# Kernel optimization log

Measured on AMD Instinct MI355X. Metric: run time of the kernel, lower is better.

Reference implementation:

```python
import jax, jax.numpy as jnp
import numpy as np

N_EMBD = 1024
HEAD_SIZE = 128
B, T = 8, 4096


def setup_inputs() -> dict:
    key = jax.random.key(0)
    ks = jax.random.split(key, 7)
    s = 1.0 / np.sqrt(N_EMBD)
    return {
        "x": jax.random.normal(ks[0], (B, T, N_EMBD), dtype=jnp.float32),
        "Wq": jax.random.uniform(ks[1], (N_EMBD, HEAD_SIZE), jnp.float32, -s, s),
        "bq": jax.random.uniform(ks[2], (HEAD_SIZE,), jnp.float32, -s, s),
        "Wk": jax.random.uniform(ks[3], (N_EMBD, HEAD_SIZE), jnp.float32, -s, s),
        "bk": jax.random.uniform(ks[4], (HEAD_SIZE,), jnp.float32, -s, s),
        "Wv": jax.random.uniform(ks[5], (N_EMBD, HEAD_SIZE), jnp.float32, -s, s),
        "bv": jax.random.uniform(ks[6], (HEAD_SIZE,), jnp.float32, -s, s),
    }


def reference(x, Wq, bq, Wk, bk, Wv, bv):
    # q,k,v: [B,T,H]
    q = x @ Wq + bq
    k = x @ Wk + bk
    v = x @ Wv + bv
    scale = HEAD_SIZE ** -0.5
    att = jnp.einsum("bth,bsh->bts", q, k) * scale  # [B,T,T]
    t = x.shape[1]
    causal = jnp.tril(jnp.ones((t, t), dtype=bool))
    att = jnp.where(causal, att, -jnp.inf)
    att = jax.nn.softmax(att, axis=-1)
    # dropout with p=0.0 is identity (eval-mode equivalent)
    out = jnp.einsum("bts,bsh->bth", att, v)  # [B,T,H]
    return out
```

## Files before the change

### kernel.cpp

```cpp
#include <hip/hip_runtime.h>
#include <hip/hip_bf16.h>
#include <stdint.h>

#define BATCH 8
#define SEQ   4096
#define EMB   1024
#define HD    128
#define NROWS 32768

typedef __attribute__((ext_vector_type(8))) short short8;
typedef __attribute__((ext_vector_type(4))) float f32x4;

__device__ inline unsigned short f2bf(float f) {
    union { float f; unsigned int u; } c; c.f = f;
    unsigned int u = c.u;
    unsigned int r = (u + 0x7fffu + ((u >> 16) & 1u)) >> 16;
    return (unsigned short)r;
}
__device__ inline float bf2f(unsigned short u) {
    union { unsigned int i; float f; } c; c.i = ((unsigned int)u) << 16; return c.f;
}
__device__ inline unsigned int pkbf(float a, float b) {
    __hip_bfloat162 h = __float22bfloat162_rn(make_float2(a, b));
    union { __hip_bfloat162 h; unsigned int u; } c; c.h = h; return c.u;
}

#define GLDS16(gp, lp) __builtin_amdgcn_global_load_lds( \
    (const __attribute__((address_space(1))) void*)(gp), \
    (__attribute__((address_space(3))) void*)(lp), 16, 0, 0)

__device__ inline void decomp(int it, int& b, int& qt, int& kv) {
    b = it / 2112;
    int r = it - b * 2112;
    int q = (int)((__builtin_sqrtf(2.0f * (float)r + 1.0f) - 1.0f) * 0.5f);
    while (2 * (q + 1) * (q + 2) <= r) ++q;
    while (2 * q * (q + 1) > r) --q;
    qt = q;
    kv = r - 2 * q * (q + 1);
}
__device__ inline int base1(int qt) {
    if (qt < 5)  return qt;
    if (qt < 11) return 5 + 2 * (qt - 5);
    if (qt < 16) return 17 + 3 * (qt - 11);
    if (qt < 22) return 32 + 4 * (qt - 16);
    if (qt < 27) return 56 + 5 * (qt - 22);
    return 81 + 6 * (qt - 27);
}

__global__ __launch_bounds__(256) void prep_kernel(
    const float* __restrict__ Wq, const float* __restrict__ bq,
    const float* __restrict__ Wk, const float* __restrict__ bk,
    const float* __restrict__ Wv, const float* __restrict__ bv,
    unsigned short* __restrict__ wt, float* __restrict__ biasc)
{
    const int n = blockIdx.x;
    const int sel = n >> 7, h = n & 127;
    const float* W = (sel == 0) ? Wq : (sel == 1) ? Wk : Wv;
    const int tid = threadIdx.x;
    const int k0 = tid * 4;
    union { unsigned short us[4]; uint2 v; } pk;
#pragma unroll
    for (int u = 0; u < 4; ++u) pk.us[u] = f2bf(W[(size_t)(k0 + u) * HD + h]);
    *(uint2*)&wt[(size_t)n * EMB + k0] = pk.v;
    if (tid == 0) {
        const float* bp = (sel == 0) ? bq : (sel == 1) ? bk : bv;
        biasc[n] = bp[h];
    }
}

__global__ __launch_bounds__(768, 3) void gemm_qkv(
    const float* __restrict__ x, const unsigned short* __restrict__ wt,
    const float* __restrict__ biasc,
    unsigned short* __restrict__ q, unsigned short* __restrict__ kOut,
    unsigned short* __restrict__ vt)
{
    const int m0  = blockIdx.x * 128;
    const int tid = threadIdx.x;
    const int wave = tid >> 6, lane = tid & 63;
    const int quad = lane >> 4, l15 = lane & 15;
    const int wm = (wave >= 6) ? 1 : 0;
    const int wn = wave - wm * 6;

    __shared__ __align__(16) unsigned short As[3][128][40];
    __shared__ __align__(16) unsigned short Bs[3][12288];

    f32x4 acc[4][4];
#pragma unroll
    for (int i = 0; i < 4; ++i)
#pragma unroll
        for (int j = 0; j < 4; ++j) acc[i][j] = (f32x4){0.f, 0.f, 0.f, 0.f};

    const int aactive = (tid < 512);
    const int arow = tid >> 3, akc = (tid & 7) * 4;
    float4 aR0, aR1;

#define LOAD_A(kt)                                                          \
    if (aactive) {                                                          \
        aR0 = *(const float4*)(x + (size_t)(m0 + arow) * EMB + (kt) * 32 + akc);        \
        aR1 = *(const float4*)(x + (size_t)(m0 + arow + 64) * EMB + (kt) * 32 + akc);   \
    }
#define WRITE_A(buf)                                                        \
    if (aactive) {                                                          \
        union { unsigned short us[4]; uint2 v; } p0, p1;                    \
        p0.us[0] = f2bf(aR0.x); p0.us[1] = f2bf(aR0.y);                     \
        p0.us[2] = f2bf(aR0.z); p0.us[3] = f2bf(aR0.w);                     \
        *(uint2*)&As[buf][arow][akc] = p0.v;                                \
        p1.us[0] = f2bf(aR1.x); p1.us[1] = f2bf(aR1.y);                     \
        p1.us[2] = f2bf(aR1.z); p1.us[3] = f2bf(aR1.w);                     \
        *(uint2*)&As[buf][arow + 64][akc] = p1.v;                           \
    }
#define STAGE_B(kt, buf)                                                    \
    {                                                                       \
        _Pragma("unroll")                                                   \
        for (int g = 0; g < 2; ++g) {                                       \
            int s0 = (g * 12 + wave) * 64;                                  \
            int s  = s0 + lane;                                             \
            int n  = s >> 2, c = (s & 3) ^ (n & 3);                         \
            GLDS16(wt + (size_t)n * EMB + (kt) * 32 + c * 8,                \
                   &Bs[buf][s0 * 8]);                                       \
        }                                                                   \
    }
#define VMW2() { asm volatile("s_waitcnt vmcnt(2)" ::: "memory"); __builtin_amdgcn_sched_barrier(0); }
#define VMW0() { asm volatile("s_waitcnt vmcnt(0)" ::: "memory"); __builtin_amdgcn_sched_barrier(0); }
#define GBAR() { asm volatile("s_waitcnt lgkmcnt(0)\n\ts_barrier" ::: "memory"); __builtin_amdgcn_sched_barrier(0); }

    LOAD_A(0);
    STAGE_B(0, 0);
    STAGE_B(1, 1);
    VMW2();
    WRITE_A(0);
    GBAR();

    int cur = 0;
    for (int kt = 0; kt < 32; ++kt) {
        if (kt < 31) LOAD_A(kt + 1);
        if (kt < 30) { int b2 = cur + 2; if (b2 >= 3) b2 -= 3; STAGE_B(kt + 2, b2); }

        short8 af[4], bw[4];
#pragma unroll
        for (int mj = 0; mj < 4; ++mj)
            af[mj] = *(const short8*)&As[cur][wm * 64 + mj * 16 + l15][quad * 8];
#pragma unroll
        for (int ni = 0; ni < 4; ++ni) {
            int n = wn * 64 + ni * 16 + l15;
            bw[ni] = *(const short8*)&Bs[cur][n * 32 + ((quad ^ (n & 3)) << 3)];
        }
#pragma unroll
        for (int ni = 0; ni < 4; ++ni)
#pragma unroll
            for (int mj = 0; mj < 4; ++mj)
                acc[ni][mj] = __builtin_amdgcn_mfma_f32_16x16x32_bf16(
                    bw[ni], af[mj], acc[ni][mj], 0, 0, 0);

        if (kt == 30) { VMW0(); } else { VMW2(); }
        if (kt < 31) {
            int nb = cur + 1; if (nb >= 3) nb -= 3;
            WRITE_A(nb);
            GBAR();
        }
        cur = (cur + 1 < 3) ? cur + 1 : 0;
    }

    const float qscale = 0.08838834764831845f * 1.4426950408889634f;
    const int bb = m0 >> 12;
    const int t0 = m0 & 4095;
    const int mrow0 = m0 + wm * 64;
    const int tl0   = t0 + wm * 64;
#pragma unroll
    for (int ni = 0; ni < 4; ++ni) {
        int colbase = wn * 64 + ni * 16;
        int sel = colbase >> 7;
        int c0 = colbase + quad * 4;
        float4 bv4 = *(const float4*)&biasc[c0];
#pragma unroll
        for (int mj = 0; mj < 4; ++mj) {
            int m = mrow0 + mj * 16 + l15;
            if (sel == 0) {
                union { unsigned short us[4]; uint2 v; } pk;
#pragma unroll
                for (int j = 0; j < 4; ++j)
                    pk.us[j] = f2bf((acc[ni][mj][j] + ((const float*)&bv4)[j]) * qscale);
                *(uint2*)&q[(size_t)m * HD + (c0 & 127)] = pk.v;
            } else if (sel == 1) {
                union { unsigned short us[4]; uint2 v; } pk;
#pragma unroll
                for (int j = 0; j < 4; ++j)
                    pk.us[j] = f2bf(acc[ni][mj][j] + ((const float*)&bv4)[j]);
                *(uint2*)&kOut[(size_t)m * HD + (c0 & 127)] = pk.v;
            } else {
#pragma unroll
                for (int j = 0; j < 4; ++j) {
                    int h = (c0 & 127) + j;
                    vt[((size_t)(bb * 128 + h)) * SEQ + tl0 + mj * 16 + l15] =
                        f2bf(acc[ni][mj][j] + ((const float*)&bv4)[j]);
                }
            }
        }
    }
#undef LOAD_A
#undef WRITE_A
#undef STAGE_B
#undef VMW2
#undef VMW0
#undef GBAR
}

__global__ __launch_bounds__(256, 3) void attn_kernel(
    const unsigned short* __restrict__ q, const unsigned short* __restrict__ k,
    const unsigned short* __restrict__ vt, float* __restrict__ out,
    float* __restrict__ Oseg, float2* __restrict__ ml)
{
    const int rank  = blockIdx.x;
    const int chunk = (rank & 7) * 96 + (rank >> 3);
    const int start = chunk * 22;
    const int iend  = start + 22;

    const int tid  = threadIdx.x;
    const int wave = tid >> 6, lane = tid & 63;
    const int quad = lane >> 4, l15 = lane & 15;

    __shared__ __align__(16) unsigned short Ks[2][4096];
    __shared__ __align__(16) unsigned short Vs[2][4096];

    const int bpa0 = (l15 + 16 * ((2 * quad) & 3)) * 4;
    const int bpa1 = (l15 + 16 * ((2 * quad + 1) & 3)) * 4;

#define STAGE_KV(b_, kv_, buf_)                                              \
    {                                                                        \
        const size_t kb0 = (size_t)(b_) * SEQ + (kv_) * 32;                  \
        const size_t vb0 = (size_t)(b_) * HD * SEQ + (kv_) * 32;             \
        _Pragma("unroll")                                                    \
        for (int g = 0; g < 2; ++g) {                                        \
            int s0 = (g * 4 + wave) * 64;                                    \
            int s  = s0 + lane;                                              \
            int key = s >> 4, c = (s & 15) ^ (key & 15);                     \
            GLDS16(k + (kb0 + key) * HD + c * 8, &Ks[buf_][s0 * 8]);         \
        }                                                                    \
        _Pragma("unroll")                                                    \
        for (int g = 0; g < 2; ++g) {                                        \
            int s0 = (g * 4 + wave) * 64;                                    \
            int s  = s0 + lane;                                              \
            int h = s >> 2, c = (s & 3) ^ ((h >> 2) & 3);                    \
            GLDS16(vt + vb0 + (size_t)h * SEQ + c * 8, &Vs[buf_][s0 * 8]);   \
        }                                                                    \
    }

    int b, qt, kv;
    decomp(start, b, qt, kv);

    short8 qf[2][4];
    f32x4  o[2][8];
    float  m_r[2], l_r[2];
    int    qrow0 = 0;

#define CTX_INIT(b_, q_)                                                     \
    {                                                                        \
        qrow0 = (q_) * 128 + wave * 32;                                      \
        const size_t qoff = (size_t)(b_) * SEQ + qrow0;                      \
        _Pragma("unroll")                                                    \
        for (int mi = 0; mi < 2; ++mi)                                       \
            _Pragma("unroll")                                                \
            for (int kh = 0; kh < 4; ++kh)                                   \
                qf[mi][kh] = *(const short8*)(q + (qoff + mi * 16 + l15) * HD + kh * 32 + quad * 8); \
        _Pragma("unroll")                                                    \
        for (int mi = 0; mi < 2; ++mi) {                                     \
            _Pragma("unroll")                                                \
            for (int hi = 0; hi < 8; ++hi) o[mi][hi] = (f32x4){0.f, 0.f, 0.f, 0.f}; \
            m_r[mi] = -1e30f; l_r[mi] = 0.f;                                 \
        }                                                                    \
    }

#define CTX_FLUSH()                                                          \
    {                                                                        \
        const int I0 = b * 2112 + 2 * qt * (qt + 1);                         \
        const int j  = chunk - I0 / 22;                                      \
        const int rr = wave * 32;                                            \
        float* obase;                                                        \
        if (j == 0) obase = out + ((size_t)b * SEQ + qrow0) * HD;            \
        else obase = Oseg + ((size_t)(b * 112 + base1(qt) + j - 1) * 128 + rr) * HD; \
        const size_t mlb = ((size_t)(b * 32 + qt) * 7 + j) * 128 + rr;       \
        _Pragma("unroll")                                                    \
        for (int mi = 0; mi < 2; ++mi) {                                     \
            if (quad == 0) ml[mlb + mi * 16 + l15] = make_float2(m_r[mi], l_r[mi]); \
            _Pragma("unroll")                                                \
            for (int hi = 0; hi < 8; ++hi)                                   \
                *(f32x4*)&obase[(size_t)(mi * 16 + l15) * HD + hi * 16 + quad * 4] = o[mi][hi]; \
        }                                                                    \
    }

#define SMAX(sarr, mi_, pk_)                                                 \
    {                                                                        \
        float mx = fmaxf(fmaxf(fmaxf(sarr[0][0], sarr[0][1]),               \
                               fmaxf(sarr[0][2], sarr[0][3])),              \
                         fmaxf(fmaxf(sarr[1][0], sarr[1][1]),               \
                               fmaxf(sarr[1][2], sarr[1][3])));             \
        mx = fmaxf(mx, __shfl_xor(mx, 16));                                  \
        mx = fmaxf(mx, __shfl_xor(mx, 32));                                  \
        if (!__all(mx - m_r[mi_] <= 8.0f)) {                                 \
            float mnew = fmaxf(m_r[mi_], mx);                                \
            float alpha = __builtin_amdgcn_exp2f(m_r[mi_] - mnew);           \
            m_r[mi_] = mnew;                                                 \
            l_r[mi_] *= alpha;                                               \
            _Pragma("unroll")                                                \
            for (int hi = 0; hi < 8; ++hi) o[mi_][hi] *= alpha;              \
        }                                                                    \
        const float mcur = m_r[mi_];                                         \
        float rs = 0.f;                                                      \
        _Pragma("unroll")                                                    \
        for (int ni = 0; ni < 2; ++ni) {                                     \
            float p0 = __builtin_amdgcn_exp2f(sarr[ni][0] - mcur);           \
            float p1 = __builtin_amdgcn_exp2f(sarr[ni][1] - mcur);           \
            float p2 = __builtin_amdgcn_exp2f(sarr[ni][2] - mcur);           \
            float p3 = __builtin_amdgcn_exp2f(sarr[ni][3] - mcur);           \
            rs += (p0 + p1) + (p2 + p3);                                     \
            pk_[ni][0] = pkbf(p0, p1);                                       \
            pk_[ni][1] = pkbf(p2, p3);                                       \
        }                                                                    \
        rs += __shfl_xor(rs, 16);                                            \
        rs += __shfl_xor(rs, 32);                                            \
        l_r[mi_] += rs;                                                      \
    }

#define BPERM(pk_, pT_)                                                      \
    {                                                                        \
        union { unsigned int u[4]; short8 s8; } pt;                          \
        unsigned int a0 = (unsigned)__builtin_amdgcn_ds_bpermute(bpa0, (int)pk_[0][0]); \
        unsigned int b0 = (unsigned)__builtin_amdgcn_ds_bpermute(bpa0, (int)pk_[1][0]); \
        pt.u[0] = (quad < 2) ? a0 : b0;                                      \
        unsigned int a1 = (unsigned)__builtin_amdgcn_ds_bpermute(bpa0, (int)pk_[0][1]); \
        unsigned int b1 = (unsigned)__builtin_amdgcn_ds_bpermute(bpa0, (int)pk_[1][1]); \
        pt.u[1] = (quad < 2) ? a1 : b1;                                      \
        unsigned int a2 = (unsigned)__builtin_amdgcn_ds_bpermute(bpa1, (int)pk_[0][0]); \
        unsigned int b2 = (unsigned)__builtin_amdgcn_ds_bpermute(bpa1, (int)pk_[1][0]); \
        pt.u[2] = (quad < 2) ? a2 : b2;                                      \
        unsigned int a3 = (unsigned)__builtin_amdgcn_ds_bpermute(bpa1, (int)pk_[0][1]); \
        unsigned int b3 = (unsigned)__builtin_amdgcn_ds_bpermute(bpa1, (int)pk_[1][1]); \
        pt.u[3] = (quad < 2) ? a3 : b3;                                      \
        pT_ = pt.s8;                                                         \
    }

    STAGE_KV(b, kv, 0);
    CTX_INIT(b, qt);
    int cur = 0;

    for (int it = start; it < iend; ++it) {
        const bool more = (it + 1 < iend);
        int b2 = b, qt2 = qt, kv2 = kv + 1;
        const bool ctxend = (kv2 == 4 * qt + 4);
        if (ctxend) { kv2 = 0; ++qt2; if (qt2 == 32) { qt2 = 0; ++b2; } }

        __syncthreads();
        if (more) STAGE_KV(b2, kv2, cur ^ 1);

        const int key0 = kv * 32;
        if (key0 <= qrow0 + 31) {
            f32x4 s0[2], s1[2];
#pragma unroll
            for (int ni = 0; ni < 2; ++ni) { s0[ni] = (f32x4){0.f,0.f,0.f,0.f}; s1[ni] = (f32x4){0.f,0.f,0.f,0.f}; }
            __builtin_amdgcn_s_setprio(1);
#pragma unroll
            for (int kh = 0; kh < 4; ++kh) {
#pragma unroll
                for (int ni = 0; ni < 2; ++ni) {
                    short8 kf = *(const short8*)&Ks[cur][(ni * 16 + l15) * 128 + (((kh * 4 + quad) ^ l15) << 3)];
                    s0[ni] = __builtin_amdgcn_mfma_f32_16x16x32_bf16(kf, qf[0][kh], s0[ni], 0, 0, 0);
                    s1[ni] = __builtin_amdgcn_mfma_f32_16x16x32_bf16(kf, qf[1][kh], s1[ni], 0, 0, 0);
                }
            }
            __builtin_amdgcn_s_setprio(0);
            if (key0 + 31 > qrow0) {
#pragma unroll
                for (int ni = 0; ni < 2; ++ni)
#pragma unroll
                    for (int j = 0; j < 4; ++j) {
                        int key = key0 + ni * 16 + quad * 4 + j;
                        if (key > qrow0 + l15)      s0[ni][j] = -1e30f;
                        if (key > qrow0 + 16 + l15) s1[ni][j] = -1e30f;
                    }
            }
            unsigned int pk0[2][2], pk1[2][2];
            short8 pT0, pT1;
            SMAX(s0, 0, pk0)
            BPERM(pk0, pT0)
            SMAX(s1, 1, pk1)
            BPERM(pk1, pT1)
            __builtin_amdgcn_s_setprio(1);
#pragma unroll
            for (int hi = 0; hi < 8; ++hi) {
                short8 vf = *(const short8*)&Vs[cur][(hi * 16 + l15) * 32 + ((quad ^ (l15 >> 2)) << 3)];
                o[0][hi] = __builtin_amdgcn_mfma_f32_16x16x32_bf16(vf, pT0, o[0][hi], 0, 0, 0);
                o[1][hi] = __builtin_amdgcn_mfma_f32_16x16x32_bf16(vf, pT1, o[1][hi], 0, 0, 0);
            }
            __builtin_amdgcn_s_setprio(0);
        }

        if (ctxend || !more) {
            CTX_FLUSH();
            if (more && ctxend) CTX_INIT(b2, qt2);
        }
        b = b2; qt = qt2; kv = kv2;
        cur ^= 1;
    }
#undef STAGE_KV
#undef CTX_INIT
#undef CTX_FLUSH
#undef SMAX
#undef BPERM
}

__global__ __launch_bounds__(256) void merge_kernel(
    float* __restrict__ out, const float* __restrict__ Oseg,
    const float2* __restrict__ ml)
{
    int idx = blockIdx.x * 256 + threadIdx.x;
    int row = idx >> 5;
    int hc  = (idx & 31) << 2;
    int b = row >> 12, t = row & 4095, qt = t >> 7, rr = t & 127;
    int I0   = b * 2112 + 2 * qt * (qt + 1);
    int n    = 4 * (qt + 1);
    int nseg = (I0 + n - 1) / 22 - I0 / 22 + 1;

    const float2* mlp = ml + ((size_t)(b * 32 + qt) * 7) * 128 + rr;
    float2 s0 = mlp[0];
    float M = s0.x;
    for (int j = 1; j < nseg; ++j) M = fmaxf(M, mlp[(size_t)j * 128].x);

    float w0 = __builtin_amdgcn_exp2f(s0.x - M);
    float L  = w0 * s0.y;
    f32x4 a = *(const f32x4*)&out[(size_t)row * HD + hc];
    a = a * w0;
    for (int j = 1; j < nseg; ++j) {
        float2 mj = mlp[(size_t)j * 128];
        float w = __builtin_amdgcn_exp2f(mj.x - M);
        L += w * mj.y;
        const float* sp = Oseg + ((size_t)(b * 112 + base1(qt) + j - 1) * 128 + rr) * HD + hc;
        f32x4 sv = *(const f32x4*)sp;
        a = a + sv * w;
    }
    float inv = 1.0f / L;
    *(f32x4*)&out[(size_t)row * HD + hc] = a * inv;
}

extern "C" void kernel_launch(void* const* d_in, const int* in_sizes, int n_in,
                              void* d_out, int out_size, void* d_ws, size_t ws_size,
                              hipStream_t stream) {
    const float* x  = (const float*)d_in[0];
    const float* Wq = (const float*)d_in[1];
    const float* bq = (const float*)d_in[2];
    const float* Wk = (const float*)d_in[3];
    const float* bk = (const float*)d_in[4];
    const float* Wv = (const float*)d_in[5];
    const float* bv = (const float*)d_in[6];
    float* out = (float*)d_out;

    unsigned short* wt    = (unsigned short*)d_ws;
    float*          biasc = (float*)((char*)d_ws + 786432);
    unsigned short* qb    = (unsigned short*)((char*)d_ws + 787968);
    unsigned short* kb    = qb  + (size_t)NROWS * HD;
    unsigned short* vtb   = kb  + (size_t)NROWS * HD;
    float*          Oseg  = (float*)((char*)d_ws + 787968 + 3ull * NROWS * HD * 2);
    float2*         mlseg = (float2*)((char*)Oseg + 896ull * 128 * HD * 4);

    prep_kernel<<<dim3(384), 256, 0, stream>>>(Wq, bq, Wk, bk, Wv, bv, wt, biasc);
    gemm_qkv<<<dim3(256), 768, 0, stream>>>(x, wt, biasc, qb, kb, vtb);
    attn_kernel<<<dim3(768), 256, 0, stream>>>(qb, kb, vtb, out, Oseg, mlseg);
    merge_kernel<<<dim3(NROWS * 32 / 256), 256, 0, stream>>>(out, Oseg, mlseg);
}
```

Baseline: 309.0 us.

## Fuse split-KV merge into attention kernel via last-block atomic counter

Removes the separate merge kernel. Query tiles covered by a single segment now normalize and write the output directly. For split tiles, each block writes its partial result, bumps a per-tile atomic counter, and the last arriving block does the log-sum-exp merge in place. This saves one kernel launch and the full read/write pass over out for single-segment tiles. In exchange it adds threadfence and syncthreads to every split flush, plus serial merge work on the tail block.

```diff
diff --git a/kernel.cpp b/kernel.cpp
--- a/kernel.cpp
+++ b/kernel.cpp
@@ -51,12 +51,14 @@
     const float* __restrict__ Wq, const float* __restrict__ bq,
     const float* __restrict__ Wk, const float* __restrict__ bk,
     const float* __restrict__ Wv, const float* __restrict__ bv,
-    unsigned short* __restrict__ wt, float* __restrict__ biasc)
+    unsigned short* __restrict__ wt, float* __restrict__ biasc,
+    int* __restrict__ cnt)
 {
     const int n = blockIdx.x;
     const int sel = n >> 7, h = n & 127;
     const float* W = (sel == 0) ? Wq : (sel == 1) ? Wk : Wv;
     const int tid = threadIdx.x;
+    if (n == 0) cnt[tid] = 0;
     const int k0 = tid * 4;
     union { unsigned short us[4]; uint2 v; } pk;
 #pragma unroll
@@ -208,7 +210,7 @@
 __global__ __launch_bounds__(256, 3) void attn_kernel(
     const unsigned short* __restrict__ q, const unsigned short* __restrict__ k,
     const unsigned short* __restrict__ vt, float* __restrict__ out,
-    float* __restrict__ Oseg, float2* __restrict__ ml)
+    float* __restrict__ Oseg, float2* __restrict__ ml, int* __restrict__ cnt)
 {
     const int rank  = blockIdx.x;
     const int chunk = (rank & 7) * 96 + (rank >> 3);
@@ -221,6 +223,7 @@
 
     __shared__ __align__(16) unsigned short Ks[2][4096];
     __shared__ __align__(16) unsigned short Vs[2][4096];
+    __shared__ int lastf;
 
     const int bpa0 = (l15 + 16 * ((2 * quad) & 3)) * 4;
     const int bpa1 = (l15 + 16 * ((2 * quad + 1) & 3)) * 4;
@@ -272,19 +275,63 @@
 
 #define CTX_FLUSH()                                                          \
     {                                                                        \
-        const int I0 = b * 2112 + 2 * qt * (qt + 1);                         \
-        const int j  = chunk - I0 / 22;                                      \
-        const int rr = wave * 32;                                            \
-        float* obase;                                                        \
-        if (j == 0) obase = out + ((size_t)b * SEQ + qrow0) * HD;            \
-        else obase = Oseg + ((size_t)(b * 112 + base1(qt) + j - 1) * 128 + rr) * HD; \
-        const size_t mlb = ((size_t)(b * 32 + qt) * 7 + j) * 128 + rr;       \
-        _Pragma("unroll")                                                    \
-        for (int mi = 0; mi < 2; ++mi) {                                     \
-            if (quad == 0) ml[mlb + mi * 16 + l15] = make_float2(m_r[mi], l_r[mi]); \
+        const int I0   = b * 2112 + 2 * qt * (qt + 1);                       \
+        const int c_lo = I0 / 22;                                            \
+        const int nseg = (I0 + 4 * (qt + 1) - 1) / 22 - c_lo + 1;            \
+        const int j    = chunk - c_lo;                                       \
+        const int rr   = wave * 32;                                          \
+        if (nseg == 1) {                                                     \
+            float* obase = out + ((size_t)b * SEQ + qrow0) * HD;             \
             _Pragma("unroll")                                                \
-            for (int hi = 0; hi < 8; ++hi)                                   \
-                *(f32x4*)&obase[(size_t)(mi * 16 + l15) * HD + hi * 16 + quad * 4] = o[mi][hi]; \
+            for (int mi = 0; mi < 2; ++mi) {                                 \
+                float inv = 1.0f / l_r[mi];                                  \
+                _Pragma("unroll")                                            \
+                for (int hi = 0; hi < 8; ++hi)                               \
+                    *(f32x4*)&obase[(size_t)(mi * 16 + l15) * HD + hi * 16 + quad * 4] = o[mi][hi] * inv; \
+            }                                                                \
+        } else {                                                             \
+            float* obase;                                                    \
+            if (j == 0) obase = out + ((size_t)b * SEQ + qrow0) * HD;        \
+            else obase = Oseg + ((size_t)(b * 112 + base1(qt) + j - 1) * 128 + rr) * HD; \
+            const size_t mlb = ((size_t)(b * 32 + qt) * 7 + j) * 128 + rr;   \
+            _Pragma("unroll")                                                \
+            for (int mi = 0; mi < 2; ++mi) {                                 \
+                if (quad == 0) ml[mlb + mi * 16 + l15] = make_float2(m_r[mi], l_r[mi]); \
+                _Pragma("unroll")                                            \
+                for (int hi = 0; hi < 8; ++hi)                               \
+                    *(f32x4*)&obase[(size_t)(mi * 16 + l15) * HD + hi * 16 + quad * 4] = o[mi][hi]; \
+            }                                                                \
+            __threadfence();                                                 \
+            __syncthreads();                                                 \
+            if (tid == 0) lastf = (atomicAdd(&cnt[b * 32 + qt], 1) == nseg - 1); \
+            __syncthreads();                                                 \
+            if (lastf) {                                                     \
+                __threadfence();                                             \
+                const size_t rowg0 = (size_t)b * SEQ + qt * 128;             \
+                const float2* mlp = ml + ((size_t)(b * 32 + qt) * 7) * 128;  \
+                const int sbase = b * 112 + base1(qt);                       \
+                for (int rep = 0; rep < 16; ++rep) {                         \
+                    int idx = rep * 256 + tid;                               \
+                    int row = idx >> 5, hcc = (idx & 31) << 2;               \
+                    float2 sv0 = mlp[row];                                   \
+                    float M = sv0.x;                                         \
+                    for (int jj = 1; jj < nseg; ++jj) M = fmaxf(M, mlp[jj * 128 + row].x); \
+                    float w0 = __builtin_amdgcn_exp2f(sv0.x - M);            \
+                    float L  = w0 * sv0.y;                                   \
+                    f32x4 a = *(f32x4*)&out[(rowg0 + row) * HD + hcc];       \
+                    a = a * w0;                                              \
+                    for (int jj = 1; jj < nseg; ++jj) {                      \
+                        float2 mj = mlp[jj * 128 + row];                     \
+                        float w = __builtin_amdgcn_exp2f(mj.x - M);          \
+                        L += w * mj.y;                                       \
+                        const float* sp = Oseg + ((size_t)(sbase + jj - 1) * 128 + row) * HD + hcc; \
+                        f32x4 sv = *(const f32x4*)sp;                        \
+                        a = a + sv * w;                                      \
+                    }                                                        \
+                    float inv = 1.0f / L;                                    \
+                    *(f32x4*)&out[(rowg0 + row) * HD + hcc] = a * inv;       \
+                }                                                            \
+            }                                                                \
         }                                                                    \
     }
 
@@ -372,10 +419,10 @@
 #pragma unroll
                 for (int ni = 0; ni < 2; ++ni)
 #pragma unroll
-                    for (int j = 0; j < 4; ++j) {
-                        int key = key0 + ni * 16 + quad * 4 + j;
-                        if (key > qrow0 + l15)      s0[ni][j] = -1e30f;
-                        if (key > qrow0 + 16 + l15) s1[ni][j] = -1e30f;
+                    for (int jj = 0; jj < 4; ++jj) {
+                        int key = key0 + ni * 16 + quad * 4 + jj;
+                        if (key > qrow0 + l15)      s0[ni][jj] = -1e30f;
+                        if (key > qrow0 + 16 + l15) s1[ni][jj] = -1e30f;
                     }
             }
             unsigned int pk0[2][2], pk1[2][2];
@@ -406,39 +453,6 @@
 #undef CTX_FLUSH
 #undef SMAX
 #undef BPERM
-}
-
-__global__ __launch_bounds__(256) void merge_kernel(
-    float* __restrict__ out, const float* __restrict__ Oseg,
-    const float2* __restrict__ ml)
-{
-    int idx = blockIdx.x * 256 + threadIdx.x;
-    int row = idx >> 5;
-    int hc  = (idx & 31) << 2;
-    int b = row >> 12, t = row & 4095, qt = t >> 7, rr = t & 127;
-    int I0   = b * 2112 + 2 * qt * (qt + 1);
-    int n    = 4 * (qt + 1);
-    int nseg = (I0 + n - 1) / 22 - I0 / 22 + 1;
-
-    const float2* mlp = ml + ((size_t)(b * 32 + qt) * 7) * 128 + rr;
-    float2 s0 = mlp[0];
-    float M = s0.x;
-    for (int j = 1; j < nseg; ++j) M = fmaxf(M, mlp[(size_t)j * 128].x);
-
-    float w0 = __builtin_amdgcn_exp2f(s0.x - M);
-    float L  = w0 * s0.y;
-    f32x4 a = *(const f32x4*)&out[(size_t)row * HD + hc];
-    a = a * w0;
-    for (int j = 1; j < nseg; ++j) {
-        float2 mj = mlp[(size_t)j * 128];
-        float w = __builtin_amdgcn_exp2f(mj.x - M);
-        L += w * mj.y;
-        const float* sp = Oseg + ((size_t)(b * 112 + base1(qt) + j - 1) * 128 + rr) * HD + hc;
-        f32x4 sv = *(const f32x4*)sp;
-        a = a + sv * w;
-    }
-    float inv = 1.0f / L;
-    *(f32x4*)&out[(size_t)row * HD + hc] = a * inv;
 }
 
 extern "C" void kernel_launch(void* const* d_in, const int* in_sizes, int n_in,
@@ -460,9 +474,9 @@
     unsigned short* vtb   = kb  + (size_t)NROWS * HD;
     float*          Oseg  = (float*)((char*)d_ws + 787968 + 3ull * NROWS * HD * 2);
     float2*         mlseg = (float2*)((char*)Oseg + 896ull * 128 * HD * 4);
-
-    prep_kernel<<<dim3(384), 256, 0, stream>>>(Wq, bq, Wk, bk, Wv, bv, wt, biasc);
+    int*            cnt   = (int*)((char*)mlseg + (size_t)BATCH * 32 * 7 * 128 * sizeof(float2));
+
+    prep_kernel<<<dim3(384), 256, 0, stream>>>(Wq, bq, Wk, bk, Wv, bv, wt, biasc, cnt);
     gemm_qkv<<<dim3(256), 768, 0, stream>>>(x, wt, biasc, qb, kb, vtb);
-    attn_kernel<<<dim3(768), 256, 0, stream>>>(qb, kb, vtb, out, Oseg, mlseg);
-    merge_kernel<<<dim3(NROWS * 32 / 256), 256, 0, stream>>>(out, Oseg, mlseg);
-}
+    attn_kernel<<<dim3(768), 256, 0, stream>>>(qb, kb, vtb, out, Oseg, mlseg, cnt);
+}
```

After: 487.6 us. +57.8%, slower.
